# Kernel optimization log

Measured on AMD Instinct MI355X. Metric: run time of the kernel, lower is better.

Reference implementation:

```python
import jax, jax.numpy as jnp
import numpy as np
from jax import lax

PC_RANGE = (-51.2, -51.2, -3.0, 51.2, 51.2, 1.0)
VOXEL = (0.4, 0.4, 4.0)
H = 256
W = 256
C = 256
EPS = 1e-5


def setup_inputs() -> dict:
    key = jax.random.key(0)
    ks = jax.random.split(key, 12)
    B, N = 4, 32
    # boxes: centers inside the BEV range with small corner offsets
    centers = jax.random.uniform(ks[0], (B, N, 1, 2), minval=-45.0, maxval=45.0)
    offsets = jax.random.normal(ks[1], (B, N, 8, 2)) * 2.0
    z = jax.random.normal(ks[2], (B, N, 8, 1))
    pred_box = jnp.concatenate([centers + offsets, z], axis=-1).astype(jnp.float32)
    pred_score = jax.random.uniform(ks[3], (B, N), dtype=jnp.float32)
    s = 0.02
    return {
        "pred_box": pred_box,
        "pred_score": pred_score,
        "W1": jax.random.normal(ks[4], (25, C), dtype=jnp.float32) * s,
        "b1": jnp.zeros((C,), jnp.float32),
        "W2": jax.random.normal(ks[5], (C, C), dtype=jnp.float32) * s,
        "b2": jnp.zeros((C,), jnp.float32),
        "W3": jax.random.normal(ks[6], (C, C), dtype=jnp.float32) * s,
        "b3": jnp.zeros((C,), jnp.float32),
        "conv_w": jax.random.normal(ks[7], (3, 2, C, C, 3, 3), dtype=jnp.float32) * s,
        "gamma": jnp.ones((3, 2, C), jnp.float32),
        "beta": jnp.zeros((3, 2, C), jnp.float32),
    }


def _conv(x, w):
    # x: [B,C,H,W], w: [O,I,3,3]
    return lax.conv_general_dilated(x, w, (1, 1), "SAME",
                                    dimension_numbers=("NCHW", "OIHW", "NCHW"))


def _bn(x, g, b):
    # BatchNorm2d in training mode; original runs with batch size 1 per CAV,
    # so stats are per-sample over (H,W). x: [B,C,H,W]
    m = x.mean(axis=(2, 3), keepdims=True)
    v = ((x - m) ** 2).mean(axis=(2, 3), keepdims=True)
    return (x - m) * jax.lax.rsqrt(v + EPS) * g[None, :, None, None] + b[None, :, None, None]


def reference(pred_box, pred_score, W1, b1, W2, b2, W3, b3, conv_w, gamma, beta):
    B, N = pred_box.shape[:2]
    xmin, ymin, _, xmax, ymax, _ = PC_RANGE
    dx, dy, _ = VOXEL

    # per-box MLP embedding
    geom = pred_box.reshape(B, N, 24)
    obj = jnp.concatenate([geom, pred_score[..., None]], axis=-1)  # [B,N,25]
    h1 = jax.nn.relu(obj @ W1 + b1)
    h2 = jax.nn.relu(h1 @ W2 + b2)
    obj_feat = (h2 @ W3 + b3) * pred_score[..., None]  # [B,N,C]

    # rasterize box AABBs onto the grid; later boxes overwrite earlier ones
    corners = pred_box[..., :2]  # [B,N,8,2]
    gx = jnp.floor((corners[..., 0] - xmin) / dx)
    gy = jnp.floor((corners[..., 1] - ymin) / dy)
    gx0 = jnp.clip(gx.min(-1), 0, W - 1).astype(jnp.int32)  # [B,N]
    gx1 = jnp.clip(gx.max(-1), 0, W - 1).astype(jnp.int32)
    gy0 = jnp.clip(gy.min(-1), 0, H - 1).astype(jnp.int32)
    gy1 = jnp.clip(gy.max(-1), 0, H - 1).astype(jnp.int32)

    xs = jnp.arange(W)
    ys = jnp.arange(H)
    mx = (xs[None, None, :] >= gx0[..., None]) & (xs[None, None, :] <= gx1[..., None])  # [B,N,W]
    my = (ys[None, None, :] >= gy0[..., None]) & (ys[None, None, :] <= gy1[..., None])  # [B,N,H]
    cover = my[:, :, :, None] & mx[:, :, None, :]  # [B,N,H,W]

    prio = jnp.arange(N, dtype=jnp.int32)[None, :, None, None]
    last = jnp.max(jnp.where(cover, prio, -1), axis=1)  # [B,H,W]: index of last covering box
    idx = jnp.clip(last, 0)
    gathered = jax.vmap(lambda of, ix: of[ix])(obj_feat, idx)  # [B,H,W,C]
    feat = jnp.where(last[..., None] >= 0, gathered, 0.0)
    x = jnp.transpose(feat, (0, 3, 1, 2))  # [B,C,H,W]

    # residual conv refine blocks
    for k in range(3):
        res = x
        y = jax.nn.relu(_bn(_conv(x, conv_w[k, 0]), gamma[k, 0], beta[k, 0]))
        y = _bn(_conv(y, conv_w[k, 1]), gamma[k, 1], beta[k, 1])
        x = jax.nn.relu(y + res)
    return x
```

## Files before the change

kernel.cpp:

```cpp
#include <hip/hip_runtime.h>
#include <hip/hip_bf16.h>

typedef short short8 __attribute__((ext_vector_type(8)));
typedef float f32x16 __attribute__((ext_vector_type(16)));

#define MFMA32 __builtin_amdgcn_mfma_f32_32x32x16_bf16
#define HWPX 65536

#define GLDS16(gp, lp) __builtin_amdgcn_global_load_lds( \
    (const __attribute__((address_space(1))) unsigned int*)(gp), \
    (__attribute__((address_space(3))) unsigned int*)(lp), 16, 0, 0)

__device__ __forceinline__ unsigned short f2bf(float f) {
  unsigned u = __float_as_uint(f);
  u += 0x7FFF + ((u >> 16) & 1);
  return (unsigned short)(u >> 16);
}
__device__ __forceinline__ float bf2f(unsigned short b) {
  return __uint_as_float(((unsigned)b) << 16);
}

__global__ void mlp_kernel(const float* __restrict__ pred_box,
                           const float* __restrict__ score,
                           const float* __restrict__ W1, const float* __restrict__ b1,
                           const float* __restrict__ W2, const float* __restrict__ b2,
                           const float* __restrict__ W3, const float* __restrict__ b3,
                           float* __restrict__ objf) {
  __shared__ float obj[25];
  __shared__ float h1[256];
  __shared__ float h2[256];
  const int box = blockIdx.x;
  const int tid = threadIdx.x;
  if (tid < 24) obj[tid] = pred_box[box * 24 + tid];
  if (tid == 24) obj[24] = score[box];
  __syncthreads();
  float acc = b1[tid];
  #pragma unroll
  for (int k = 0; k < 25; ++k) acc = fmaf(obj[k], W1[k * 256 + tid], acc);
  h1[tid] = fmaxf(acc, 0.f);
  __syncthreads();
  acc = b2[tid];
  #pragma unroll 8
  for (int k = 0; k < 256; ++k) acc = fmaf(h1[k], W2[k * 256 + tid], acc);
  h2[tid] = fmaxf(acc, 0.f);
  __syncthreads();
  acc = b3[tid];
  #pragma unroll 8
  for (int k = 0; k < 256; ++k) acc = fmaf(h2[k], W3[k * 256 + tid], acc);
  objf[box * 256 + tid] = acc * score[box];
}

__global__ void bounds_kernel(const float* __restrict__ pred_box,
                              int* __restrict__ bnds) {
  const int t = threadIdx.x;
  const float* p = pred_box + t * 24;
  float gx0 = 1e30f, gx1 = -1e30f, gy0 = 1e30f, gy1 = -1e30f;
  #pragma unroll
  for (int j = 0; j < 8; ++j) {
    float gx = floorf((p[j * 3 + 0] + 51.2f) / 0.4f);
    float gy = floorf((p[j * 3 + 1] + 51.2f) / 0.4f);
    gx0 = fminf(gx0, gx); gx1 = fmaxf(gx1, gx);
    gy0 = fminf(gy0, gy); gy1 = fmaxf(gy1, gy);
  }
  bnds[t * 4 + 0] = (int)fminf(fmaxf(gx0, 0.f), 255.f);
  bnds[t * 4 + 1] = (int)fminf(fmaxf(gx1, 0.f), 255.f);
  bnds[t * 4 + 2] = (int)fminf(fmaxf(gy0, 0.f), 255.f);
  bnds[t * 4 + 3] = (int)fminf(fmaxf(gy1, 0.f), 255.f);
}

__global__ void wt_kernel(const float* __restrict__ w, unsigned short* __restrict__ wt) {
  int i = blockIdx.x * 256 + threadIdx.x;
  int j = i & 7;
  int l = (i >> 3) & 63;
  int nb = (i >> 9) & 7;
  int ks = (i >> 12) & 15;
  int t2 = i >> 16;
  int tap = t2 % 9;
  int cv = t2 / 9;
  int co = nb * 32 + (l & 31);
  int ci = ks * 16 + ((l >> 5) << 3) + j;
  wt[i] = f2bf(w[(size_t)((cv * 256 + co) * 256 + ci) * 9 + tap]);
}

__global__ void raster_nhwc(const int* __restrict__ bnds,
                            const float* __restrict__ objf,
                            unsigned short* __restrict__ xB) {
  const int y = blockIdx.x;
  const int b = blockIdx.y;
  const int x = threadIdx.x;
  __shared__ int sb[128];
  __shared__ int lastA[256];
  if (x < 128) sb[x] = bnds[b * 128 + x];
  __syncthreads();
  int last = -1;
  #pragma unroll
  for (int n = 0; n < 32; ++n) {
    int bx0 = sb[n * 4 + 0], bx1 = sb[n * 4 + 1];
    int by0 = sb[n * 4 + 2], by1 = sb[n * 4 + 3];
    if (x >= bx0 && x <= bx1 && y >= by0 && y <= by1) last = n;
  }
  lastA[x] = last;
  __syncthreads();
  unsigned short* row = xB + ((size_t)b * HWPX + y * 256) * 256;
  for (int it = 0; it < 32; ++it) {
    int s = x + 256 * it;
    int px = s >> 5;
    int c8 = (s & 31) * 8;
    int ln = lastA[px];
    short8 v = {0, 0, 0, 0, 0, 0, 0, 0};
    if (ln >= 0) {
      const float* f = objf + (b * 32 + ln) * 256 + c8;
      #pragma unroll
      for (int j = 0; j < 8; ++j) v[j] = (short)f2bf(f[j]);
    }
    *(short8*)(row + px * 256 + c8) = v;
  }
}

__global__ __launch_bounds__(256, 2) void conv_mfma(const unsigned short* __restrict__ in,
                                                    const unsigned short* __restrict__ wt,
                                                    const unsigned short* __restrict__ zbuf,
                                                    unsigned short* __restrict__ T,
                                                    float* __restrict__ part) {
  __shared__ unsigned short lds[2][16 * 528];
  const int bid0 = blockIdx.x;
  const int swz = (bid0 & 7) * 256 + (bid0 >> 3);
  const int b = swz >> 9;
  const int bid = swz & 511;
  const int x0 = (bid & 3) * 64;
  const int y0 = (bid >> 2) * 2;
  const int tid = threadIdx.x;
  const int lane = tid & 63;
  const int wid = tid >> 6;
  const int h = lane >> 5;
  const int l31 = lane & 31;
  const int col0 = l31 * 8;

  const unsigned short* inb = in + (size_t)b * (HWPX * 256);
  unsigned short* Tb = T + (size_t)b * (HWPX * 256);

  f32x16 acc[4][2];
  #pragma unroll
  for (int a = 0; a < 4; ++a)
    #pragma unroll
    for (int n = 0; n < 2; ++n)
      #pragma unroll
      for (int r = 0; r < 16; ++r) acc[a][n][r] = 0.f;

  const unsigned short* wbase = wt + (size_t)(wid * 2) * 512 + lane * 8;

  short8 edgev;

  auto stage = [&](int c1, int buf) {
    const int ci0 = c1 * 32;
    #pragma unroll
    for (int i = 0; i < 4; ++i) {
      const int rowg = wid * 4 + i;
      const int row = rowg >> 2;
      const int g = rowg & 3;
      const int yg = y0 + row - 1;
      unsigned short* lp = &lds[buf][((row << 2) | ((g & 1) << 1) | (g >> 1)) * 528 + 8];
      const unsigned short* gp;
      if ((unsigned)yg < 256u)
        gp = inb + ((size_t)(yg * 256 + x0 + lane) * 256 + ci0 + g * 8);
      else
        gp = zbuf + lane * 8;
      GLDS16(gp, lp);
    }
  };

  auto edge_load = [&](int c1) {
    edgev = (short8){0, 0, 0, 0, 0, 0, 0, 0};
    if (tid < 32) {
      int row = tid >> 3, side = (tid >> 2) & 1, g = tid & 3;
      int yg = y0 + row - 1;
      int xg = x0 + (side ? 64 : -1);
      if ((unsigned)yg < 256u && (unsigned)xg < 256u)
        edgev = *(const short8*)(inb + ((size_t)(yg * 256 + xg) * 256 + c1 * 32 + g * 8));
    }
  };
  auto edge_store = [&](int buf) {
    if (tid < 32) {
      int row = tid >> 3, side = (tid >> 2) & 1, g = tid & 3;
      *(short8*)&lds[buf][((row << 2) | ((g & 1) << 1) | (g >> 1)) * 528 + (side ? 65 : 0) * 8] = edgev;
    }
  };

  #define LOADA(s, d) { \
    const int ks_ = (s) / 9, tap_ = (s) % 9, ky_ = tap_ / 3, kx_ = tap_ % 3; \
    const unsigned short* p_ = lbase + ky_ * 2112 + ks_ * 528 + kx_ * 8 + col0; \
    d[0] = *(const short8*)(p_); \
    d[1] = *(const short8*)(p_ + 256); \
    d[2] = *(const short8*)(p_ + 2112); \
    d[3] = *(const short8*)(p_ + 2368); }

  #define LOADB(s, d) { \
    const unsigned short* p_ = wbase + (size_t)((((s) % 9) * 16 + c * 2 + (s) / 9) * 8) * 512; \
    d[0] = *(const short8*)(p_); d[1] = *(const short8*)(p_ + 512); }

  auto compute = [&](int buf, int c) {
    const unsigned short* lbase = &lds[buf][0] + h * 1056;
    short8 Af[2][4];
    short8 Bf[3][2];
    LOADA(0, Af[0]);
    LOADB(0, Bf[0]);
    LOADB(1, Bf[1]);
    #pragma unroll
    for (int s = 0; s < 18; ++s) {
      if (s + 2 < 18) LOADB(s + 2, Bf[(s + 2) % 3]);
      if (s + 1 < 18) LOADA(s + 1, Af[(s + 1) & 1]);
      __builtin_amdgcn_s_setprio(1);
      #pragma unroll
      for (int mf = 0; mf < 4; ++mf)
        #pragma unroll
        for (int nf = 0; nf < 2; ++nf)
          acc[mf][nf] = MFMA32(Af[s & 1][mf], Bf[s % 3][nf], acc[mf][nf], 0, 0, 0);
      __builtin_amdgcn_s_setprio(0);
    }
  };

  stage(0, 0);
  edge_load(0);
  edge_store(0);
  asm volatile("s_waitcnt lgkmcnt(0)" ::: "memory");

  int cur = 0;
  for (int c = 0; c < 8; ++c) {
    if (c < 7) {
      stage(c + 1, cur ^ 1);
      asm volatile("s_waitcnt vmcnt(4)" ::: "memory");
    } else {
      asm volatile("s_waitcnt vmcnt(0)" ::: "memory");
    }
    __builtin_amdgcn_s_barrier();
    if (c < 7) edge_load(c + 1);
    compute(cur, c);
    if (c < 7) edge_store(cur ^ 1);
    asm volatile("s_waitcnt lgkmcnt(0)" ::: "memory");
    __builtin_amdgcn_s_barrier();
    cur ^= 1;
  }

  #pragma unroll
  for (int mf = 0; mf < 4; ++mf)
    #pragma unroll
    for (int nf = 0; nf < 2; ++nf) {
      unsigned short* o = Tb + ((size_t)((y0 + (mf >> 1)) * 256) + x0 + (mf & 1) * 32) * 256
                          + wid * 64 + nf * 32 + l31;
      #pragma unroll
      for (int r = 0; r < 16; ++r) {
        int m = (r & 3) + 8 * (r >> 2) + 4 * h;
        o[(size_t)m * 256] = f2bf(acc[mf][nf][r]);
      }
    }
  #pragma unroll
  for (int nf = 0; nf < 2; ++nf) {
    float s = 0.f, s2 = 0.f;
    #pragma unroll
    for (int mf = 0; mf < 4; ++mf)
      #pragma unroll
      for (int r = 0; r < 16; ++r) {
        float v = acc[mf][nf][r];
        s += v; s2 += v * v;
      }
    s += __shfl_xor(s, 32);
    s2 += __shfl_xor(s2, 32);
    if (lane < 32) {
      part[((size_t)swz * 256 + wid * 64 + nf * 32 + lane) * 2] = s;
      part[((size_t)swz * 256 + wid * 64 + nf * 32 + lane) * 2 + 1] = s2;
    }
  }
  #undef LOADA
  #undef LOADB
}

__global__ void stats2(const float* __restrict__ part,
                       const float* __restrict__ g, const float* __restrict__ be,
                       float* __restrict__ sc, float* __restrict__ sh) {
  const int ch = blockIdx.x;
  const int b = blockIdx.y;
  const int t = threadIdx.x;
  double s = 0.0, s2 = 0.0;
  #pragma unroll
  for (int i = 0; i < 2; ++i) {
    int p = b * 512 + t + i * 256;
    s += (double)part[((size_t)p * 256 + ch) * 2];
    s2 += (double)part[((size_t)p * 256 + ch) * 2 + 1];
  }
  #pragma unroll
  for (int off = 32; off > 0; off >>= 1) {
    s += __shfl_down(s, off);
    s2 += __shfl_down(s2, off);
  }
  __shared__ double ls[4], ls2[4];
  if ((t & 63) == 0) { ls[t >> 6] = s; ls2[t >> 6] = s2; }
  __syncthreads();
  if (t == 0) {
    double S = ls[0] + ls[1] + ls[2] + ls[3];
    double S2 = ls2[0] + ls2[1] + ls2[2] + ls2[3];
    double m = S / 65536.0;
    double var = S2 / 65536.0 - m * m;
    double inv = 1.0 / sqrt(var + 1e-5);
    float scv = (float)inv * g[ch];
    sc[b * 256 + ch] = scv;
    sh[b * 256 + ch] = be[ch] - (float)m * scv;
  }
}

__global__ void bnrelu(const unsigned short* __restrict__ T,
                       const float* __restrict__ sc, const float* __restrict__ sh,
                       unsigned short* __restrict__ yB) {
  #pragma unroll
  for (int it = 0; it < 8; ++it) {
    size_t e = (size_t)it * 1048576 + blockIdx.x * 256 + threadIdx.x;
    int b = (int)(e >> 21);
    int ch8 = (int)(e & 31);
    const float* scp = sc + b * 256 + ch8 * 8;
    const float* shp = sh + b * 256 + ch8 * 8;
    float4 s0 = ((const float4*)scp)[0], s1 = ((const float4*)scp)[1];
    float4 h0 = ((const float4*)shp)[0], h1 = ((const float4*)shp)[1];
    float scv[8] = {s0.x, s0.y, s0.z, s0.w, s1.x, s1.y, s1.z, s1.w};
    float shv[8] = {h0.x, h0.y, h0.z, h0.w, h1.x, h1.y, h1.z, h1.w};
    short8 v = ((const short8*)T)[e];
    short8 o;
    #pragma unroll
    for (int j = 0; j < 8; ++j)
      o[j] = (short)f2bf(fmaxf(fmaf(bf2f((unsigned short)v[j]), scv[j], shv[j]), 0.f));
    ((short8*)yB)[e] = o;
  }
}

__global__ void bnres(const unsigned short* __restrict__ T,
                      const float* __restrict__ sc, const float* __restrict__ sh,
                      unsigned short* __restrict__ xB) {
  #pragma unroll
  for (int it = 0; it < 8; ++it) {
    size_t e = (size_t)it * 1048576 + blockIdx.x * 256 + threadIdx.x;
    int b = (int)(e >> 21);
    int ch8 = (int)(e & 31);
    const float* scp = sc + b * 256 + ch8 * 8;
    const float* shp = sh + b * 256 + ch8 * 8;
    float4 s0 = ((const float4*)scp)[0], s1 = ((const float4*)scp)[1];
    float4 h0 = ((const float4*)shp)[0], h1 = ((const float4*)shp)[1];
    float scv[8] = {s0.x, s0.y, s0.z, s0.w, s1.x, s1.y, s1.z, s1.w};
    float shv[8] = {h0.x, h0.y, h0.z, h0.w, h1.x, h1.y, h1.z, h1.w};
    short8 v = ((const short8*)T)[e];
    short8 rb = ((const short8*)xB)[e];
    short8 o;
    #pragma unroll
    for (int j = 0; j < 8; ++j) {
      float f = fmaf(bf2f((unsigned short)v[j]), scv[j], shv[j]) + bf2f((unsigned short)rb[j]);
      o[j] = (short)f2bf(fmaxf(f, 0.f));
    }
    ((short8*)xB)[e] = o;
  }
}

__global__ void bnres_tr(const unsigned short* __restrict__ T,
                         const float* __restrict__ sc, const float* __restrict__ sh,
                         const unsigned short* __restrict__ xB,
                         float* __restrict__ out) {
  __shared__ float tl[64][65];
  const int pxb = blockIdx.x >> 2;
  const int chb = blockIdx.x & 3;
  const int b = blockIdx.y;
  const int px0 = pxb * 64;
  const int ch0 = chb * 64;
  const int tid = threadIdx.x;
  #pragma unroll
  for (int i = 0; i < 2; ++i) {
    int p = (tid >> 3) + 32 * i;
    int c8 = (tid & 7) * 8;
    size_t e = ((size_t)b * HWPX + px0 + p) * 256 + ch0 + c8;
    const float* scp = sc + b * 256 + ch0 + c8;
    const float* shp = sh + b * 256 + ch0 + c8;
    float4 s0 = ((const float4*)scp)[0], s1 = ((const float4*)scp)[1];
    float4 h0 = ((const float4*)shp)[0], h1 = ((const float4*)shp)[1];
    float scv[8] = {s0.x, s0.y, s0.z, s0.w, s1.x, s1.y, s1.z, s1.w};
    float shv[8] = {h0.x, h0.y, h0.z, h0.w, h1.x, h1.y, h1.z, h1.w};
    short8 v = *(const short8*)(T + e);
    short8 rb = *(const short8*)(xB + e);
    #pragma unroll
    for (int j = 0; j < 8; ++j) {
      float f = fmaf(bf2f((unsigned short)v[j]), scv[j], shv[j]) + bf2f((unsigned short)rb[j]);
      tl[p][c8 + j] = fmaxf(f, 0.f);
    }
  }
  __syncthreads();
  float* ob = out + (size_t)b * (HWPX * 256);
  #pragma unroll
  for (int i = 0; i < 16; ++i) {
    int c = (tid >> 6) + 4 * i;
    int p = tid & 63;
    ob[(size_t)(ch0 + c) * HWPX + px0 + p] = tl[p][c];
  }
}

extern "C" void kernel_launch(void* const* d_in, const int* in_sizes, int n_in,
                              void* d_out, int out_size, void* d_ws, size_t ws_size,
                              hipStream_t stream) {
  const float* pred_box   = (const float*)d_in[0];
  const float* pred_score = (const float*)d_in[1];
  const float* W1 = (const float*)d_in[2];
  const float* b1 = (const float*)d_in[3];
  const float* W2 = (const float*)d_in[4];
  const float* b2 = (const float*)d_in[5];
  const float* W3 = (const float*)d_in[6];
  const float* b3 = (const float*)d_in[7];
  const float* conv_w = (const float*)d_in[8];
  const float* gamma  = (const float*)d_in[9];
  const float* beta   = (const float*)d_in[10];
  float* out = (float*)d_out;

  char* wsb = (char*)d_ws;
  float* objf = (float*)(wsb + 0);
  int*   bnds = (int*)(wsb + 0x40000);
  float* sc   = (float*)(wsb + 0x42000);
  float* sh   = (float*)(wsb + 0x44000);
  float* part = (float*)(wsb + 0x100000);
  unsigned short* zbuf = (unsigned short*)(wsb + 0x500000);
  unsigned short* wtAll = (unsigned short*)(wsb + 0x600000);
  unsigned short* xB = (unsigned short*)(wsb + (size_t)16 * 1024 * 1024);
  unsigned short* yB = (unsigned short*)(wsb + (size_t)160 * 1024 * 1024);
  unsigned short* T  = (unsigned short*)(wsb + (size_t)304 * 1024 * 1024);

  hipMemsetAsync(zbuf, 0, 4096, stream);
  mlp_kernel<<<128, 256, 0, stream>>>(pred_box, pred_score, W1, b1, W2, b2, W3, b3, objf);
  bounds_kernel<<<1, 128, 0, stream>>>(pred_box, bnds);
  wt_kernel<<<13824, 256, 0, stream>>>(conv_w, wtAll);
  raster_nhwc<<<dim3(256, 4), 256, 0, stream>>>(bnds, objf, xB);

  for (int k = 0; k < 3; ++k) {
    const unsigned short* wk0 = wtAll + (size_t)(k * 2 + 0) * 589824;
    const unsigned short* wk1 = wtAll + (size_t)(k * 2 + 1) * 589824;
    conv_mfma<<<2048, 256, 0, stream>>>(xB, wk0, zbuf, T, part);
    stats2<<<dim3(256, 4), 256, 0, stream>>>(part, gamma + (k * 2 + 0) * 256,
                                             beta + (k * 2 + 0) * 256, sc, sh);
    bnrelu<<<4096, 256, 0, stream>>>(T, sc, sh, yB);
    conv_mfma<<<2048, 256, 0, stream>>>(yB, wk1, zbuf, T, part);
    stats2<<<dim3(256, 4), 256, 0, stream>>>(part, gamma + (k * 2 + 1) * 256,
                                             beta + (k * 2 + 1) * 256, sc, sh);
    if (k < 2)
      bnres<<<4096, 256, 0, stream>>>(T, sc, sh, xB);
    else
      bnres_tr<<<dim3(4096, 4), 256, 0, stream>>>(T, sc, sh, xB, out);
  }
}
```

Baseline: 1.962 ms.

## Split conv output channels across two blocks to shrink accumulators and raise occupancy

Each conv block now covers half of the output channels, and each wave computes a 64-pixel by 64-channel tile instead of 128x64. This halves the accumulator registers, which allows three blocks per CU instead of two, and doubles the grid to 4096 blocks. The partial-statistics layout and the stats reduction are widened to match. In exchange every input tile is staged into LDS twice (once per channel half), which doubles input global traffic and per-MFMA LDS A-reads.

```diff
diff --git a/kernel.cpp b/kernel.cpp
--- a/kernel.cpp
+++ b/kernel.cpp
@@ -117,21 +117,26 @@
   }
 }
 
-__global__ __launch_bounds__(256, 2) void conv_mfma(const unsigned short* __restrict__ in,
+__global__ __launch_bounds__(256, 3) void conv_mfma(const unsigned short* __restrict__ in,
                                                     const unsigned short* __restrict__ wt,
                                                     const unsigned short* __restrict__ zbuf,
                                                     unsigned short* __restrict__ T,
                                                     float* __restrict__ part) {
   __shared__ unsigned short lds[2][16 * 528];
   const int bid0 = blockIdx.x;
-  const int swz = (bid0 & 7) * 256 + (bid0 >> 3);
-  const int b = swz >> 9;
-  const int bid = swz & 511;
-  const int x0 = (bid & 3) * 64;
-  const int y0 = (bid >> 2) * 2;
+  const int swz = (bid0 & 7) * 512 + (bid0 >> 3);
+  const int b = swz >> 10;
+  const int r = swz & 1023;
+  const int cop = r >> 9;
+  const int yt = (r >> 2) & 127;
+  const int xt = r & 3;
+  const int x0 = xt * 64;
+  const int y0 = yt * 2;
   const int tid = threadIdx.x;
   const int lane = tid & 63;
   const int wid = tid >> 6;
+  const int pxh = wid >> 1;
+  const int coq = wid & 1;
   const int h = lane >> 5;
   const int l31 = lane & 31;
   const int col0 = l31 * 8;
@@ -139,15 +144,15 @@
   const unsigned short* inb = in + (size_t)b * (HWPX * 256);
   unsigned short* Tb = T + (size_t)b * (HWPX * 256);
 
-  f32x16 acc[4][2];
-  #pragma unroll
-  for (int a = 0; a < 4; ++a)
+  f32x16 acc[2][2];
+  #pragma unroll
+  for (int a = 0; a < 2; ++a)
     #pragma unroll
     for (int n = 0; n < 2; ++n)
       #pragma unroll
-      for (int r = 0; r < 16; ++r) acc[a][n][r] = 0.f;
-
-  const unsigned short* wbase = wt + (size_t)(wid * 2) * 512 + lane * 8;
+      for (int q = 0; q < 16; ++q) acc[a][n][q] = 0.f;
+
+  const unsigned short* wbase = wt + (size_t)(cop * 4 + coq * 2) * 512 + lane * 8;
 
   short8 edgev;
 
@@ -190,17 +195,15 @@
     const int ks_ = (s) / 9, tap_ = (s) % 9, ky_ = tap_ / 3, kx_ = tap_ % 3; \
     const unsigned short* p_ = lbase + ky_ * 2112 + ks_ * 528 + kx_ * 8 + col0; \
     d[0] = *(const short8*)(p_); \
-    d[1] = *(const short8*)(p_ + 256); \
-    d[2] = *(const short8*)(p_ + 2112); \
-    d[3] = *(const short8*)(p_ + 2368); }
+    d[1] = *(const short8*)(p_ + 256); }
 
   #define LOADB(s, d) { \
     const unsigned short* p_ = wbase + (size_t)((((s) % 9) * 16 + c * 2 + (s) / 9) * 8) * 512; \
     d[0] = *(const short8*)(p_); d[1] = *(const short8*)(p_ + 512); }
 
   auto compute = [&](int buf, int c) {
-    const unsigned short* lbase = &lds[buf][0] + h * 1056;
-    short8 Af[2][4];
+    const unsigned short* lbase = &lds[buf][0] + pxh * 2112 + h * 1056;
+    short8 Af[2][2];
     short8 Bf[3][2];
     LOADA(0, Af[0]);
     LOADB(0, Bf[0]);
@@ -210,11 +213,10 @@
       if (s + 2 < 18) LOADB(s + 2, Bf[(s + 2) % 3]);
       if (s + 1 < 18) LOADA(s + 1, Af[(s + 1) & 1]);
       __builtin_amdgcn_s_setprio(1);
-      #pragma unroll
-      for (int mf = 0; mf < 4; ++mf)
-        #pragma unroll
-        for (int nf = 0; nf < 2; ++nf)
-          acc[mf][nf] = MFMA32(Af[s & 1][mf], Bf[s % 3][nf], acc[mf][nf], 0, 0, 0);
+      acc[0][0] = MFMA32(Af[s & 1][0], Bf[s % 3][0], acc[0][0], 0, 0, 0);
+      acc[0][1] = MFMA32(Af[s & 1][0], Bf[s % 3][1], acc[0][1], 0, 0, 0);
+      acc[1][0] = MFMA32(Af[s & 1][1], Bf[s % 3][0], acc[1][0], 0, 0, 0);
+      acc[1][1] = MFMA32(Af[s & 1][1], Bf[s % 3][1], acc[1][1], 0, 0, 0);
       __builtin_amdgcn_s_setprio(0);
     }
   };
@@ -242,32 +244,34 @@
   }
 
   #pragma unroll
-  for (int mf = 0; mf < 4; ++mf)
+  for (int mf = 0; mf < 2; ++mf)
     #pragma unroll
     for (int nf = 0; nf < 2; ++nf) {
-      unsigned short* o = Tb + ((size_t)((y0 + (mf >> 1)) * 256) + x0 + (mf & 1) * 32) * 256
-                          + wid * 64 + nf * 32 + l31;
+      unsigned short* o = Tb + ((size_t)((y0 + pxh) * 256) + x0 + mf * 32) * 256
+                          + cop * 128 + coq * 64 + nf * 32 + l31;
       #pragma unroll
-      for (int r = 0; r < 16; ++r) {
-        int m = (r & 3) + 8 * (r >> 2) + 4 * h;
-        o[(size_t)m * 256] = f2bf(acc[mf][nf][r]);
+      for (int q = 0; q < 16; ++q) {
+        int m = (q & 3) + 8 * (q >> 2) + 4 * h;
+        o[(size_t)m * 256] = f2bf(acc[mf][nf][q]);
       }
     }
+  const int slot = (b * 512 + yt * 4 + xt) * 2 + pxh;
   #pragma unroll
   for (int nf = 0; nf < 2; ++nf) {
     float s = 0.f, s2 = 0.f;
     #pragma unroll
-    for (int mf = 0; mf < 4; ++mf)
+    for (int mf = 0; mf < 2; ++mf)
       #pragma unroll
-      for (int r = 0; r < 16; ++r) {
-        float v = acc[mf][nf][r];
+      for (int q = 0; q < 16; ++q) {
+        float v = acc[mf][nf][q];
         s += v; s2 += v * v;
       }
     s += __shfl_xor(s, 32);
     s2 += __shfl_xor(s2, 32);
     if (lane < 32) {
-      part[((size_t)swz * 256 + wid * 64 + nf * 32 + lane) * 2] = s;
-      part[((size_t)swz * 256 + wid * 64 + nf * 32 + lane) * 2 + 1] = s2;
+      size_t idx = (size_t)slot * 256 + cop * 128 + coq * 64 + nf * 32 + lane;
+      part[idx * 2] = s;
+      part[idx * 2 + 1] = s2;
     }
   }
   #undef LOADA
@@ -282,8 +286,8 @@
   const int t = threadIdx.x;
   double s = 0.0, s2 = 0.0;
   #pragma unroll
-  for (int i = 0; i < 2; ++i) {
-    int p = b * 512 + t + i * 256;
+  for (int i = 0; i < 4; ++i) {
+    int p = b * 1024 + t + i * 256;
     s += (double)part[((size_t)p * 256 + ch) * 2];
     s2 += (double)part[((size_t)p * 256 + ch) * 2 + 1];
   }
@@ -417,9 +421,9 @@
   int*   bnds = (int*)(wsb + 0x40000);
   float* sc   = (float*)(wsb + 0x42000);
   float* sh   = (float*)(wsb + 0x44000);
-  float* part = (float*)(wsb + 0x100000);
-  unsigned short* zbuf = (unsigned short*)(wsb + 0x500000);
-  unsigned short* wtAll = (unsigned short*)(wsb + 0x600000);
+  unsigned short* zbuf = (unsigned short*)(wsb + 0x48000);
+  unsigned short* wtAll = (unsigned short*)(wsb + 0x100000);
+  float* part = (float*)(wsb + 0x800000);
   unsigned short* xB = (unsigned short*)(wsb + (size_t)16 * 1024 * 1024);
   unsigned short* yB = (unsigned short*)(wsb + (size_t)160 * 1024 * 1024);
   unsigned short* T  = (unsigned short*)(wsb + (size_t)304 * 1024 * 1024);
@@ -433,11 +437,11 @@
   for (int k = 0; k < 3; ++k) {
     const unsigned short* wk0 = wtAll + (size_t)(k * 2 + 0) * 589824;
     const unsigned short* wk1 = wtAll + (size_t)(k * 2 + 1) * 589824;
-    conv_mfma<<<2048, 256, 0, stream>>>(xB, wk0, zbuf, T, part);
+    conv_mfma<<<4096, 256, 0, stream>>>(xB, wk0, zbuf, T, part);
     stats2<<<dim3(256, 4), 256, 0, stream>>>(part, gamma + (k * 2 + 0) * 256,
                                              beta + (k * 2 + 0) * 256, sc, sh);
     bnrelu<<<4096, 256, 0, stream>>>(T, sc, sh, yB);
-    conv_mfma<<<2048, 256, 0, stream>>>(yB, wk1, zbuf, T, part);
+    conv_mfma<<<4096, 256, 0, stream>>>(yB, wk1, zbuf, T, part);
     stats2<<<dim3(256, 4), 256, 0, stream>>>(part, gamma + (k * 2 + 1) * 256,
                                              beta + (k * 2 + 1) * 256, sc, sh);
     if (k < 2)
```

Result: slower. 2.322 ms (+18.3%).
